# Optimization experiments

Measured on AMD Instinct MI355X. Metric: run time of the kernel, lower is better.

Reference implementation:

```python
import jax, jax.numpy as jnp
import numpy as np

LN_EPS = 1e-5

def layer_norm(x, w, b):
    m = jnp.mean(x, axis=-1, keepdims=True)
    v = jnp.mean((x - m) ** 2, axis=-1, keepdims=True)
    return (x - m) * jax.lax.rsqrt(v + LN_EPS) * w + b

def setup_inputs() -> dict:
    key = jax.random.key(0)
    ks = jax.random.split(key, 10)
    B, N, L = 32, 576, 100
    low, high = 1024, 1536
    inp = {
        "vit_feat": jax.random.normal(ks[0], (B, N, low), dtype=jnp.float32),
        "box_feat": jax.random.normal(ks[1], (B, L, high), dtype=jnp.float32),
        "lengths": jax.random.randint(ks[2], (B,), 0, L, dtype=jnp.int64),
        # query projector: LayerNorm(low) + Linear(low, low)
        "q_ln_w": jnp.ones((low,), jnp.float32),
        "q_ln_b": jnp.zeros((low,), jnp.float32),
        "q_w": jax.random.normal(ks[3], (low, low), dtype=jnp.float32) * 0.02,
        "q_b": jnp.zeros((low,), jnp.float32),
        # key projector: LayerNorm(high) + Linear(high, low)
        "k_ln_w": jnp.ones((high,), jnp.float32),
        "k_ln_b": jnp.zeros((high,), jnp.float32),
        "k_w": jax.random.normal(ks[4], (high, low), dtype=jnp.float32) * 0.02,
        "k_b": jnp.zeros((low,), jnp.float32),
        # value projector: LayerNorm(high) + Linear(high, low)
        "v_ln_w": jnp.ones((high,), jnp.float32),
        "v_ln_b": jnp.zeros((high,), jnp.float32),
        "v_w": jax.random.normal(ks[5], (high, low), dtype=jnp.float32) * 0.02,
        "v_b": jnp.zeros((low,), jnp.float32),
    }
    return inp

def reference(vit_feat, box_feat, lengths,
              q_ln_w, q_ln_b, q_w, q_b,
              k_ln_w, k_ln_b, k_w, k_b,
              v_ln_w, v_ln_b, v_w, v_b):
    B, L = box_feat.shape[0], box_feat.shape[1]
    # padding mask, same as the original per-row copy loop
    mask = jnp.arange(L)[None, :] < lengths[:, None]          # [B, L] bool
    q = layer_norm(vit_feat, q_ln_w, q_ln_b) @ q_w + q_b      # [B, N, low]
    k = layer_norm(box_feat, k_ln_w, k_ln_b) @ k_w + k_b      # [B, L, low]
    v = layer_norm(box_feat, v_ln_w, v_ln_b) @ v_w + v_b      # [B, L, low]
    scale = 1.0 / jnp.sqrt(jnp.asarray(k.shape[-1], q.dtype))
    att = jnp.einsum('bnd,bld->bnl', q, k * scale)            # [B, N, L]
    att = jnp.where(mask[:, None, :], att, -jnp.inf)
    att = jnp.nan_to_num(att)  # -inf -> finite min, matching torch nan_to_num
    att = jax.nn.softmax(att, axis=-1)
    out = jnp.einsum('bnl,bld->bnd', att, v)                  # [B, N, low]
    return vit_feat + out
```

## Files before the change

kernel.cpp:

```cpp
#include <hip/hip_runtime.h>
#include <stdint.h>

typedef __attribute__((ext_vector_type(8))) short short8;
typedef __attribute__((ext_vector_type(4))) float f32x4;

#define NEG_FLT_MAX (-3.402823466e38f)

__device__ __forceinline__ unsigned short f2bf(float f) {
  uint32_t u = __float_as_uint(f);
  uint32_t r = (u + 0x7fffu + ((u >> 16) & 1u)) >> 16;
  return (unsigned short)r;
}

__device__ __forceinline__ void gload16(const void* g, void* l) {
  __builtin_amdgcn_global_load_lds(
      (const __attribute__((address_space(1))) uint32_t*)g,
      (__attribute__((address_space(3))) uint32_t*)l, 16, 0, 0);
}

__global__ __launch_bounds__(256) void prep_kernel(
    const float* __restrict__ qw, const float* __restrict__ kw,
    const float* __restrict__ vw, const float* __restrict__ qb,
    const float* __restrict__ kb, float scale,
    unsigned short* __restrict__ qwb, unsigned short* __restrict__ kwb,
    unsigned short* __restrict__ vwt,
    float* __restrict__ bias3, float* __restrict__ w4, float* __restrict__ c4) {
  __shared__ float tile[32][33];
  const int bid = blockIdx.x;
  const int t = threadIdx.x;
  if (bid < 2560) {
    const int idx = bid * 256 + t;
    const int QG = 1024 * 1024 / 4;
    if (idx < QG) {
      float4 v = ((const float4*)qw)[idx];
      ushort4 o;
      o.x = f2bf(v.x); o.y = f2bf(v.y); o.z = f2bf(v.z); o.w = f2bf(v.w);
      ((ushort4*)qwb)[idx] = o;
    } else {
      const int j = idx - QG;
      float4 v = ((const float4*)kw)[j];
      ushort4 o;
      o.x = f2bf(v.x * scale); o.y = f2bf(v.y * scale);
      o.z = f2bf(v.z * scale); o.w = f2bf(v.w * scale);
      ((ushort4*)kwb)[j] = o;
    }
  } else if (bid < 4096) {
    const int j = bid - 2560;
    const int c0 = (j & 31) * 32, r0 = (j >> 5) * 32;
    const int tx = t & 31, ty = t >> 5;
#pragma unroll
    for (int i = ty; i < 32; i += 8)
      tile[i][tx] = vw[(size_t)(r0 + i) * 1024 + (c0 + tx)];
    __syncthreads();
#pragma unroll
    for (int i = ty; i < 32; i += 8)
      vwt[(size_t)(c0 + i) * 1536 + (r0 + tx)] = f2bf(tile[tx][i]);
  } else {
    const int idx = bid - 4096;
    const int wv = t >> 6, l = t & 63;
    float s = 0.f;
    if (idx < 256) {
      const int i = idx * 4 + wv;
      const float* row = qw + (size_t)i * 1024;
#pragma unroll
      for (int s0 = 0; s0 < 1024; s0 += 256) {
        float4 a = *(const float4*)(row + s0 + l * 4);
        float4 b = *(const float4*)(kb + s0 + l * 4);
        s += a.x * b.x + a.y * b.y + a.z * b.z + a.w * b.w;
      }
#pragma unroll
      for (int off = 32; off; off >>= 1) s += __shfl_xor(s, off);
      if (l == 0) bias3[i] = s * scale;
    } else if (idx < 640) {
      const int j = (idx - 256) * 4 + wv;
      const float* row = kw + (size_t)j * 1024;
#pragma unroll
      for (int s0 = 0; s0 < 1024; s0 += 256) {
        float4 a = *(const float4*)(row + s0 + l * 4);
        float4 b = *(const float4*)(qb + s0 + l * 4);
        s += a.x * b.x + a.y * b.y + a.z * b.z + a.w * b.w;
      }
#pragma unroll
      for (int off = 32; off; off >>= 1) s += __shfl_xor(s, off);
      if (l == 0) w4[j] = s * scale;
    } else if (wv == 0) {
#pragma unroll
      for (int s0 = 0; s0 < 1024; s0 += 256) {
        float4 a = *(const float4*)(qb + s0 + l * 4);
        float4 b = *(const float4*)(kb + s0 + l * 4);
        s += a.x * b.x + a.y * b.y + a.z * b.z + a.w * b.w;
      }
#pragma unroll
      for (int off = 32; off; off >>= 1) s += __shfl_xor(s, off);
      if (l == 0) *c4 = s * scale;
    }
  }
}

__device__ __forceinline__ void gemm_core64(
    const unsigned short* __restrict__ A, int lda, int rowmaxA, int tm0,
    const unsigned short* __restrict__ Bt, int ldb, int rowmaxB, int tn0,
    int K, unsigned short* As, unsigned short* Bs, f32x4 acc[4][4]) {
  const int tid = threadIdx.x;
  const int w = tid >> 6, l = tid & 63;
  const int wr = w >> 1, wc = w & 1;
  const int srow = (w << 4) + (l >> 2);
  const int scol = (l & 3) << 3;
  int ra0 = tm0 + srow;      if (ra0 > rowmaxA) ra0 = rowmaxA;
  int ra1 = tm0 + srow + 64; if (ra1 > rowmaxA) ra1 = rowmaxA;
  int rb0 = tn0 + srow;      if (rb0 > rowmaxB) rb0 = rowmaxB;
  int rb1 = tn0 + srow + 64; if (rb1 > rowmaxB) rb1 = rowmaxB;
  const unsigned short* pa0 = A + (size_t)ra0 * lda + scol;
  const unsigned short* pa1 = A + (size_t)ra1 * lda + scol;
  const unsigned short* pb0 = Bt + (size_t)rb0 * ldb + scol;
  const unsigned short* pb1 = Bt + (size_t)rb1 * ldb + scol;
  unsigned short* la0 = As + (w << 4) * 32;
  unsigned short* la1 = As + ((w << 4) + 64) * 32;
  unsigned short* lb0 = Bs + (w << 4) * 32;
  unsigned short* lb1 = Bs + ((w << 4) + 64) * 32;
  const int foff = ((l & 15) << 5) + ((l >> 4) << 3);
  const unsigned short* fa = As + (wr << 6) * 32 + foff;
  const unsigned short* fb = Bs + (wc << 6) * 32 + foff;
#pragma unroll
  for (int i = 0; i < 4; i++)
#pragma unroll
    for (int j = 0; j < 4; j++) acc[i][j] = (f32x4)0.0f;
  for (int k0 = 0; k0 < K; k0 += 64) {
    gload16(pa0 + k0, la0);
    gload16(pa1 + k0, la1);
    gload16(pb0 + k0, lb0);
    gload16(pb1 + k0, lb1);
    gload16(pa0 + k0 + 32, la0 + 4096);
    gload16(pa1 + k0 + 32, la1 + 4096);
    gload16(pb0 + k0 + 32, lb0 + 4096);
    gload16(pb1 + k0 + 32, lb1 + 4096);
    __syncthreads();
    {
      short8 a[4], b[4];
#pragma unroll
      for (int i = 0; i < 4; i++) a[i] = *(const short8*)(fa + i * 512);
#pragma unroll
      for (int j = 0; j < 4; j++) b[j] = *(const short8*)(fb + j * 512);
#pragma unroll
      for (int i = 0; i < 4; i++)
#pragma unroll
        for (int j = 0; j < 4; j++)
          acc[i][j] = __builtin_amdgcn_mfma_f32_16x16x32_bf16(a[i], b[j], acc[i][j], 0, 0, 0);
    }
    {
      short8 a[4], b[4];
#pragma unroll
      for (int i = 0; i < 4; i++) a[i] = *(const short8*)(fa + 4096 + i * 512);
#pragma unroll
      for (int j = 0; j < 4; j++) b[j] = *(const short8*)(fb + 4096 + j * 512);
#pragma unroll
      for (int i = 0; i < 4; i++)
#pragma unroll
        for (int j = 0; j < 4; j++)
          acc[i][j] = __builtin_amdgcn_mfma_f32_16x16x32_bf16(a[i], b[j], acc[i][j], 0, 0, 0);
    }
    __syncthreads();
  }
}

__global__ __launch_bounds__(256) void mid_kernel(
    const float* __restrict__ box,
    const float* __restrict__ klnw, const float* __restrict__ klnb,
    const float* __restrict__ vlnw, const float* __restrict__ vlnb,
    const unsigned short* __restrict__ qwb, const unsigned short* __restrict__ kwb,
    const float* __restrict__ w4v, const float* __restrict__ c4,
    unsigned short* __restrict__ kn, unsigned short* __restrict__ vn,
    unsigned short* __restrict__ W3, float* __restrict__ qbk) {
  __shared__ float red[8];
  __shared__ float redq[4];
  __shared__ unsigned short As[128 * 64];
  __shared__ unsigned short Bs[128 * 64];
  const int t = threadIdx.x;
  if (blockIdx.x < 3200) {
    const int row = blockIdx.x;
    const float4* xr = (const float4*)(box + (size_t)row * 1536);
    const float4 a = xr[t];
    float4 c = make_float4(0.f, 0.f, 0.f, 0.f);
    if (t < 128) c = xr[256 + t];
    float s = a.x + a.y + a.z + a.w + c.x + c.y + c.z + c.w;
    float ss = a.x * a.x + a.y * a.y + a.z * a.z + a.w * a.w +
               c.x * c.x + c.y * c.y + c.z * c.z + c.w * c.w;
#pragma unroll
    for (int off = 32; off > 0; off >>= 1) {
      s += __shfl_xor(s, off);
      ss += __shfl_xor(ss, off);
    }
    if ((t & 63) == 0) { red[(t >> 6) * 2] = s; red[(t >> 6) * 2 + 1] = ss; }
    __syncthreads();
    if (t == 0) {
      float aa = 0.f, bb = 0.f;
      for (int i = 0; i < 4; i++) { aa += red[i * 2]; bb += red[i * 2 + 1]; }
      red[0] = aa; red[1] = bb;
    }
    __syncthreads();
    s = red[0]; ss = red[1];
    const float m = s * (1.f / 1536.f);
    const float var = ss * (1.f / 1536.f) - m * m;
    const float rstd = rsqrtf(var + 1e-5f);
    float qd;
    {
      const float4 w4 = ((const float4*)klnw)[t];
      const float4 b4 = ((const float4*)klnb)[t];
      const float k0v = (a.x - m) * rstd * w4.x + b4.x;
      const float k1v = (a.y - m) * rstd * w4.y + b4.y;
      const float k2v = (a.z - m) * rstd * w4.z + b4.z;
      const float k3v = (a.w - m) * rstd * w4.w + b4.w;
      ushort4 o;
      o.x = f2bf(k0v); o.y = f2bf(k1v); o.z = f2bf(k2v); o.w = f2bf(k3v);
      ((ushort4*)(kn + (size_t)row * 1536))[t] = o;
      const float4 wq = ((const float4*)w4v)[t];
      qd = k0v * wq.x + k1v * wq.y + k2v * wq.z + k3v * wq.w;
      const float4 w4vv = ((const float4*)vlnw)[t];
      const float4 b4vv = ((const float4*)vlnb)[t];
      o.x = f2bf((a.x - m) * rstd * w4vv.x + b4vv.x);
      o.y = f2bf((a.y - m) * rstd * w4vv.y + b4vv.y);
      o.z = f2bf((a.z - m) * rstd * w4vv.z + b4vv.z);
      o.w = f2bf((a.w - m) * rstd * w4vv.w + b4vv.w);
      ((ushort4*)(vn + (size_t)row * 1536))[t] = o;
    }
    if (t < 128) {
      const int t2 = 256 + t;
      const float4 w4 = ((const float4*)klnw)[t2];
      const float4 b4 = ((const float4*)klnb)[t2];
      const float k0v = (c.x - m) * rstd * w4.x + b4.x;
      const float k1v = (c.y - m) * rstd * w4.y + b4.y;
      const float k2v = (c.z - m) * rstd * w4.z + b4.z;
      const float k3v = (c.w - m) * rstd * w4.w + b4.w;
      ushort4 o;
      o.x = f2bf(k0v); o.y = f2bf(k1v); o.z = f2bf(k2v); o.w = f2bf(k3v);
      ((ushort4*)(kn + (size_t)row * 1536))[t2] = o;
      const float4 wq = ((const float4*)w4v)[t2];
      qd += k0v * wq.x + k1v * wq.y + k2v * wq.z + k3v * wq.w;
      const float4 w4vv = ((const float4*)vlnw)[t2];
      const float4 b4vv = ((const float4*)vlnb)[t2];
      o.x = f2bf((c.x - m) * rstd * w4vv.x + b4vv.x);
      o.y = f2bf((c.y - m) * rstd * w4vv.y + b4vv.y);
      o.z = f2bf((c.z - m) * rstd * w4vv.z + b4vv.z);
      o.w = f2bf((c.w - m) * rstd * w4vv.w + b4vv.w);
      ((ushort4*)(vn + (size_t)row * 1536))[t2] = o;
    }
#pragma unroll
    for (int off = 32; off; off >>= 1) qd += __shfl_xor(qd, off);
    if ((t & 63) == 0) redq[t >> 6] = qd;
    __syncthreads();
    if (t == 0) qbk[row] = redq[0] + redq[1] + redq[2] + redq[3] + c4[0];
  } else {
    const int j = blockIdx.x - 3200;
    const int tm0 = (j & 7) * 128, tn0 = (j >> 3) * 128;
    f32x4 acc[4][4];
    gemm_core64(qwb, 1024, 1023, tm0, kwb, 1024, 1535, tn0, 1024, As, Bs, acc);
    const int w = t >> 6, l = t & 63;
    const int wr = w >> 1, wc = w & 1;
#pragma unroll
    for (int i = 0; i < 4; i++) {
      const int row0 = tm0 + wr * 64 + i * 16 + (l >> 4) * 4;
#pragma unroll
      for (int jj = 0; jj < 4; jj++) {
        const int col = tn0 + wc * 64 + jj * 16 + (l & 15);
#pragma unroll
        for (int r = 0; r < 4; r++)
          W3[(size_t)(row0 + r) * 1536 + col] = f2bf(acc[i][jj][r]);
      }
    }
  }
}

__global__ __launch_bounds__(256) void gemm_kv_kernel(
    const unsigned short* __restrict__ kn, const unsigned short* __restrict__ vn,
    const unsigned short* __restrict__ W3, const unsigned short* __restrict__ vwt,
    const float* __restrict__ bias3, const float* __restrict__ vb,
    unsigned short* __restrict__ kq, unsigned short* __restrict__ vT) {
  __shared__ unsigned short As[128 * 64];
  __shared__ unsigned short Bs[128 * 64];
  const int id = blockIdx.x;
  const int sw = (id & 7) * 50 + (id >> 3);
  const int z = sw / 200;
  const int rem = sw - z * 200;
  const int tm0 = (rem % 25) * 128, tn0 = (rem / 25) * 128;
  const unsigned short* A = z ? vn : kn;
  const unsigned short* Bt = z ? vwt : W3;
  const float* bias = z ? vb : bias3;
  f32x4 acc[4][4];
  gemm_core64(A, 1536, 3199, tm0, Bt, 1536, 1023, tn0, 1536, As, Bs, acc);
  const int tid = threadIdx.x;
  const int w = tid >> 6, l = tid & 63;
  const int wr = w >> 1, wc = w & 1;
#pragma unroll
  for (int i = 0; i < 4; i++) {
    const int row0 = tm0 + wr * 64 + i * 16 + (l >> 4) * 4;
#pragma unroll
    for (int j = 0; j < 4; j++) {
      const int col = tn0 + wc * 64 + j * 16 + (l & 15);
      const float bv = bias[col];
#pragma unroll
      for (int r = 0; r < 4; r++) {
        const int row = row0 + r;
        const float val = acc[i][j][r] + bv;
        if (!z) {
          kq[(size_t)row * 1024 + col] = f2bf(val);
        } else {
          const int bb = row / 100;
          const int ll = row - bb * 100;
          vT[((size_t)bb * 1024 + col) * 128 + ll] = f2bf(val);
        }
      }
    }
  }
}

__device__ __forceinline__ void block_reduce2(float& s, float& ss, float* red) {
#pragma unroll
  for (int off = 32; off > 0; off >>= 1) {
    s += __shfl_xor(s, off);
    ss += __shfl_xor(ss, off);
  }
  const int wave = threadIdx.x >> 6;
  const int lane = threadIdx.x & 63;
  if (lane == 0) { red[wave * 2] = s; red[wave * 2 + 1] = ss; }
  __syncthreads();
  if (threadIdx.x == 0) {
    float a = 0.f, b = 0.f;
    for (int i = 0; i < 4; i++) { a += red[i * 2]; b += red[i * 2 + 1]; }
    red[0] = a; red[1] = b;
  }
  __syncthreads();
  s = red[0]; ss = red[1];
}

__global__ __launch_bounds__(256) void ln_vit_kernel(
    const float* __restrict__ x, const float* __restrict__ w,
    const float* __restrict__ b, unsigned short* __restrict__ out) {
  __shared__ float red[8];
  const int row = blockIdx.x;
  const int t = threadIdx.x;
  const float4 v = ((const float4*)(x + (size_t)row * 1024))[t];
  float s = v.x + v.y + v.z + v.w;
  float ss = v.x * v.x + v.y * v.y + v.z * v.z + v.w * v.w;
  block_reduce2(s, ss, red);
  const float m = s * (1.f / 1024.f);
  const float var = ss * (1.f / 1024.f) - m * m;
  const float rstd = rsqrtf(var + 1e-5f);
  const float4 w4 = ((const float4*)w)[t];
  const float4 b4 = ((const float4*)b)[t];
  ushort4 o;
  o.x = f2bf((v.x - m) * rstd * w4.x + b4.x);
  o.y = f2bf((v.y - m) * rstd * w4.y + b4.y);
  o.z = f2bf((v.z - m) * rstd * w4.z + b4.z);
  o.w = f2bf((v.w - m) * rstd * w4.w + b4.w);
  ((ushort4*)(out + (size_t)row * 1024))[t] = o;
}

__global__ __launch_bounds__(256) void attfused_kernel(
    const unsigned short* __restrict__ qn, const unsigned short* __restrict__ kq,
    const unsigned short* __restrict__ vT, const float* __restrict__ qbk,
    const int* __restrict__ lengths, const float* __restrict__ vit,
    float* __restrict__ out) {
  __shared__ __align__(16) char smem[45824];
  float* Smat = (float*)smem;
  float* invr = (float*)(smem + 28672);
  float* qb_l = (float*)(smem + 28800);
  const int PB = 20480, BV = 29440;

  const int b = blockIdx.y;
  const int tm0 = blockIdx.x * 32;
  const int t = threadIdx.x;
  const int w = t >> 6, l = t & 63;
  const int lo = l & 15, hi = l >> 4;
  if (t < 128) qb_l[t] = (t < 100) ? qbk[b * 100 + t] : 0.f;

  const unsigned short* A = qn + (size_t)b * 576 * 1024;
  const unsigned short* B = kq + (size_t)b * 100 * 1024;
  const int ar = (t & 127) >> 2, ah = t >> 7, ac = (t & 3) << 3;
  const unsigned short* paA = A + (size_t)(tm0 + ar) * 1024 + ah * 32 + ac;
  const unsigned short* pbB[4];
#pragma unroll
  for (int i = 0; i < 4; i++) {
    int rb = (i & 1) * 64 + (t >> 2); if (rb > 99) rb = 99;
    pbB[i] = B + (size_t)rb * 1024 + (i >> 1) * 32 + ((t & 3) << 3);
  }
  const int cw = w << 5;

  f32x4 acc[2][2];
#pragma unroll
  for (int i = 0; i < 2; i++) { acc[i][0] = (f32x4)0.0f; acc[i][1] = (f32x4)0.0f; }

  for (int k0 = 0; k0 < 1024; k0 += 64) {
    gload16(paA + k0, smem + w * 1024);
#pragma unroll
    for (int i = 0; i < 4; i++)
      gload16(pbB[i] + k0, smem + 4096 + i * 4096 + w * 1024);
    __syncthreads();
#pragma unroll
    for (int half = 0; half < 2; half++) {
      short8 a[2], bb[2];
#pragma unroll
      for (int i = 0; i < 2; i++)
        a[i] = *(const short8*)(smem + half * 2048 + (i * 16 + lo) * 64 + hi * 16);
#pragma unroll
      for (int j = 0; j < 2; j++)
        bb[j] = *(const short8*)(smem + 4096 + half * 8192 + (cw + j * 16 + lo) * 64 + hi * 16);
#pragma unroll
      for (int i = 0; i < 2; i++)
#pragma unroll
        for (int j = 0; j < 2; j++)
          acc[i][j] = __builtin_amdgcn_mfma_f32_16x16x32_bf16(a[i], bb[j], acc[i][j], 0, 0, 0);
    }
    __syncthreads();
  }

#pragma unroll
  for (int i = 0; i < 2; i++) {
    const int r0 = i * 16 + hi * 4;
#pragma unroll
    for (int j = 0; j < 2; j++) {
      const int c = cw + j * 16 + lo;
      const float qb = qb_l[c];
#pragma unroll
      for (int rr = 0; rr < 4; rr++) Smat[c * 36 + r0 + rr] = acc[i][j][rr] + qb;
    }
  }
  __syncthreads();

  const int r = t >> 3, g = t & 7;
  const int len = lengths[b];
  float mx = NEG_FLT_MAX;
#pragma unroll
  for (int i = 0; i < 13; i++) {
    const int ll = g * 13 + i;
    if (ll < 100) {
      const float v = (ll < len) ? Smat[ll * 36 + r] : NEG_FLT_MAX;
      mx = fmaxf(mx, v);
    }
  }
  mx = fmaxf(mx, __shfl_xor(mx, 1));
  mx = fmaxf(mx, __shfl_xor(mx, 2));
  mx = fmaxf(mx, __shfl_xor(mx, 4));
  float sum = 0.f;
#pragma unroll
  for (int i = 0; i < 13; i++) {
    const int ll = g * 13 + i;
    if (ll < 100) {
      const float v = (ll < len) ? Smat[ll * 36 + r] : NEG_FLT_MAX;
      const float e = __expf(v - mx);
      Smat[ll * 36 + r] = e;
      sum += e;
    }
  }
  sum += __shfl_xor(sum, 1);
  sum += __shfl_xor(sum, 2);
  sum += __shfl_xor(sum, 4);
  if (g == 0) invr[r] = 1.f / sum;
  __syncthreads();

  {
    const float inv = invr[r];
#pragma unroll
    for (int jj = 0; jj < 4; jj++) {
      const int c0 = g * 16 + jj * 4;
      ushort4 o;
      o.x = (c0 + 0 < 100) ? f2bf(Smat[(c0 + 0) * 36 + r] * inv) : (unsigned short)0;
      o.y = (c0 + 1 < 100) ? f2bf(Smat[(c0 + 1) * 36 + r] * inv) : (unsigned short)0;
      o.z = (c0 + 2 < 100) ? f2bf(Smat[(c0 + 2) * 36 + r] * inv) : (unsigned short)0;
      o.w = (c0 + 3 < 100) ? f2bf(Smat[(c0 + 3) * 36 + r] * inv) : (unsigned short)0;
      const int phys = (r * 256 + g * 32 + jj * 8) ^ ((r & 7) << 4);
      *(ushort4*)(smem + PB + phys) = o;
    }
  }
  __syncthreads();

  const unsigned short* vTb = vT + (size_t)b * 131072;
  const float* vitb = vit + ((size_t)b * 576 + tm0) * 1024;
  float* outb = out + ((size_t)b * 576 + tm0) * 1024;
  const int sBcol = ((t & 15) ^ ((t >> 4) & 7)) << 3;
  for (int nt = 0; nt < 16; ++nt) {
#pragma unroll
    for (int i = 0; i < 4; i++) {
      const int vrow = nt * 64 + i * 16 + (t >> 4);
      gload16(vTb + (size_t)vrow * 128 + sBcol, smem + BV + i * 4096 + w * 1024);
    }
    __syncthreads();
    f32x4 acc2[2];
    acc2[0] = (f32x4)0.0f; acc2[1] = (f32x4)0.0f;
#pragma unroll
    for (int ks = 0; ks < 4; ks++) {
      short8 av[2], bv;
#pragma unroll
      for (int i = 0; i < 2; i++) {
        const int m = i * 16 + lo;
        av[i] = *(const short8*)(smem + PB + ((m * 256 + ks * 64 + hi * 16) ^ ((m & 7) << 4)));
      }
      const int n = (w << 4) + lo;
      bv = *(const short8*)(smem + BV + ((n * 256 + ks * 64 + hi * 16) ^ ((n & 7) << 4)));
      acc2[0] = __builtin_amdgcn_mfma_f32_16x16x32_bf16(av[0], bv, acc2[0], 0, 0, 0);
      acc2[1] = __builtin_amdgcn_mfma_f32_16x16x32_bf16(av[1], bv, acc2[1], 0, 0, 0);
    }
#pragma unroll
    for (int i = 0; i < 2; i++) {
      const int col = (w << 4) + lo;
#pragma unroll
      for (int rr = 0; rr < 4; rr++) {
        const int row = i * 16 + hi * 4 + rr;
        *(float*)(smem + ((row * 256 + col * 4) ^ ((row & 7) << 4))) = acc2[i][rr];
      }
    }
    __syncthreads();
#pragma unroll
    for (int m = 0; m < 2; m++) {
      const int row = m * 16 + (t >> 4);
      const int colb = (t & 15) * 4;
      float4 e = *(const float4*)(smem + ((row * 256 + colb * 4) ^ ((row & 7) << 4)));
      const size_t gidx = (size_t)row * 1024 + nt * 64 + colb;
      float4 vv = *(const float4*)(vitb + gidx);
      e.x += vv.x; e.y += vv.y; e.z += vv.z; e.w += vv.w;
      *(float4*)(outb + gidx) = e;
    }
    __syncthreads();
  }
}

extern "C" void kernel_launch(void* const* d_in, const int* in_sizes, int n_in,
                              void* d_out, int out_size, void* d_ws, size_t ws_size,
                              hipStream_t stream) {
  const float* vit = (const float*)d_in[0];
  const float* box = (const float*)d_in[1];
  const int* lengths = (const int*)d_in[2];
  const float* q_ln_w = (const float*)d_in[3];
  const float* q_ln_b = (const float*)d_in[4];
  const float* q_w = (const float*)d_in[5];
  const float* q_b = (const float*)d_in[6];
  const float* k_ln_w = (const float*)d_in[7];
  const float* k_ln_b = (const float*)d_in[8];
  const float* k_w = (const float*)d_in[9];
  const float* k_b = (const float*)d_in[10];
  const float* v_ln_w = (const float*)d_in[11];
  const float* v_ln_b = (const float*)d_in[12];
  const float* v_w = (const float*)d_in[13];
  const float* v_b = (const float*)d_in[14];
  float* out = (float*)d_out;
  char* ws = (char*)d_ws;

  unsigned short* kn    = (unsigned short*)(ws + 0);
  unsigned short* vn    = (unsigned short*)(ws + 9830400);
  unsigned short* v_wt  = (unsigned short*)(ws + 19660800);
  unsigned short* qwb   = (unsigned short*)(ws + 22806528);
  unsigned short* kwb   = (unsigned short*)(ws + 24903680);
  unsigned short* W3    = (unsigned short*)(ws + 28049408);
  float*          bias3 = (float*)(ws + 31195136);
  float*          w4    = (float*)(ws + 31199232);
  float*          c4    = (float*)(ws + 31207424);
  unsigned short* qn    = (unsigned short*)(ws + 0);
  float*          qbk   = (float*)(ws + 37748736);
  unsigned short* kq    = (unsigned short*)(ws + 37761536);
  unsigned short* vT    = (unsigned short*)(ws + 44315136);

  const float scale = 0.03125f;

  prep_kernel<<<4737, 256, 0, stream>>>(q_w, k_w, v_w, q_b, k_b, scale,
                                        qwb, kwb, v_wt, bias3, w4, c4);

  mid_kernel<<<3296, 256, 0, stream>>>(box, k_ln_w, k_ln_b, v_ln_w, v_ln_b,
                                       qwb, kwb, w4, c4, kn, vn, W3, qbk);

  gemm_kv_kernel<<<400, 256, 0, stream>>>(kn, vn, W3, v_wt, bias3, v_b, kq, vT);

  ln_vit_kernel<<<18432, 256, 0, stream>>>(vit, q_ln_w, q_ln_b, qn);

  attfused_kernel<<<dim3(18, 32), 256, 0, stream>>>(
      qn, kq, vT, qbk, lengths, vit, out);

  (void)in_sizes; (void)n_in; (void)out_size; (void)ws_size;
}
```

Baseline: 153.3 us.

## Merge weight prep into LayerNorm kernel and move qbk dot into KV GEMM launch

Removes the separate weight-prep kernel. The q_w/k_w bf16 conversion now happens inside the W3 GEMM tiles, with fp32 loaded and converted on the fly into LDS, and the v_w transpose and bias dots run as extra block ranges of one large kernel alongside the box LayerNorm. The per-row qbk dot product, previously fused into LayerNorm, now runs in extra blocks of the K/V GEMM kernel, reading bf16 kn. This cuts one launch and the intermediate qwb/kwb buffers. In exchange the W3 GEMM loses its async global-to-LDS loads, and qbk is computed from rounded bf16 activations.

```diff
diff --git a/kernel.cpp b/kernel.cpp
--- a/kernel.cpp
+++ b/kernel.cpp
@@ -12,89 +12,14 @@
   return (unsigned short)r;
 }
 
+__device__ __forceinline__ float bf2f(unsigned short u) {
+  return __uint_as_float(((uint32_t)u) << 16);
+}
+
 __device__ __forceinline__ void gload16(const void* g, void* l) {
   __builtin_amdgcn_global_load_lds(
       (const __attribute__((address_space(1))) uint32_t*)g,
       (__attribute__((address_space(3))) uint32_t*)l, 16, 0, 0);
-}
-
-__global__ __launch_bounds__(256) void prep_kernel(
-    const float* __restrict__ qw, const float* __restrict__ kw,
-    const float* __restrict__ vw, const float* __restrict__ qb,
-    const float* __restrict__ kb, float scale,
-    unsigned short* __restrict__ qwb, unsigned short* __restrict__ kwb,
-    unsigned short* __restrict__ vwt,
-    float* __restrict__ bias3, float* __restrict__ w4, float* __restrict__ c4) {
-  __shared__ float tile[32][33];
-  const int bid = blockIdx.x;
-  const int t = threadIdx.x;
-  if (bid < 2560) {
-    const int idx = bid * 256 + t;
-    const int QG = 1024 * 1024 / 4;
-    if (idx < QG) {
-      float4 v = ((const float4*)qw)[idx];
-      ushort4 o;
-      o.x = f2bf(v.x); o.y = f2bf(v.y); o.z = f2bf(v.z); o.w = f2bf(v.w);
-      ((ushort4*)qwb)[idx] = o;
-    } else {
-      const int j = idx - QG;
-      float4 v = ((const float4*)kw)[j];
-      ushort4 o;
-      o.x = f2bf(v.x * scale); o.y = f2bf(v.y * scale);
-      o.z = f2bf(v.z * scale); o.w = f2bf(v.w * scale);
-      ((ushort4*)kwb)[j] = o;
-    }
-  } else if (bid < 4096) {
-    const int j = bid - 2560;
-    const int c0 = (j & 31) * 32, r0 = (j >> 5) * 32;
-    const int tx = t & 31, ty = t >> 5;
-#pragma unroll
-    for (int i = ty; i < 32; i += 8)
-      tile[i][tx] = vw[(size_t)(r0 + i) * 1024 + (c0 + tx)];
-    __syncthreads();
-#pragma unroll
-    for (int i = ty; i < 32; i += 8)
-      vwt[(size_t)(c0 + i) * 1536 + (r0 + tx)] = f2bf(tile[tx][i]);
-  } else {
-    const int idx = bid - 4096;
-    const int wv = t >> 6, l = t & 63;
-    float s = 0.f;
-    if (idx < 256) {
-      const int i = idx * 4 + wv;
-      const float* row = qw + (size_t)i * 1024;
-#pragma unroll
-      for (int s0 = 0; s0 < 1024; s0 += 256) {
-        float4 a = *(const float4*)(row + s0 + l * 4);
-        float4 b = *(const float4*)(kb + s0 + l * 4);
-        s += a.x * b.x + a.y * b.y + a.z * b.z + a.w * b.w;
-      }
-#pragma unroll
-      for (int off = 32; off; off >>= 1) s += __shfl_xor(s, off);
-      if (l == 0) bias3[i] = s * scale;
-    } else if (idx < 640) {
-      const int j = (idx - 256) * 4 + wv;
-      const float* row = kw + (size_t)j * 1024;
-#pragma unroll
-      for (int s0 = 0; s0 < 1024; s0 += 256) {
-        float4 a = *(const float4*)(row + s0 + l * 4);
-        float4 b = *(const float4*)(qb + s0 + l * 4);
-        s += a.x * b.x + a.y * b.y + a.z * b.z + a.w * b.w;
-      }
-#pragma unroll
-      for (int off = 32; off; off >>= 1) s += __shfl_xor(s, off);
-      if (l == 0) w4[j] = s * scale;
-    } else if (wv == 0) {
-#pragma unroll
-      for (int s0 = 0; s0 < 1024; s0 += 256) {
-        float4 a = *(const float4*)(qb + s0 + l * 4);
-        float4 b = *(const float4*)(kb + s0 + l * 4);
-        s += a.x * b.x + a.y * b.y + a.z * b.z + a.w * b.w;
-      }
-#pragma unroll
-      for (int off = 32; off; off >>= 1) s += __shfl_xor(s, off);
-      if (l == 0) *c4 = s * scale;
-    }
-  }
 }
 
 __device__ __forceinline__ void gemm_core64(
@@ -163,21 +88,22 @@
   }
 }
 
-__global__ __launch_bounds__(256) void mid_kernel(
+__global__ __launch_bounds__(256) void mega_kernel(
     const float* __restrict__ box,
     const float* __restrict__ klnw, const float* __restrict__ klnb,
     const float* __restrict__ vlnw, const float* __restrict__ vlnb,
-    const unsigned short* __restrict__ qwb, const unsigned short* __restrict__ kwb,
-    const float* __restrict__ w4v, const float* __restrict__ c4,
+    const float* __restrict__ qw, const float* __restrict__ kw,
+    const float* __restrict__ vw, const float* __restrict__ qb,
+    const float* __restrict__ kb, float scale,
     unsigned short* __restrict__ kn, unsigned short* __restrict__ vn,
-    unsigned short* __restrict__ W3, float* __restrict__ qbk) {
-  __shared__ float red[8];
-  __shared__ float redq[4];
-  __shared__ unsigned short As[128 * 64];
-  __shared__ unsigned short Bs[128 * 64];
+    unsigned short* __restrict__ W3, unsigned short* __restrict__ vwt,
+    float* __restrict__ bias3, float* __restrict__ w4, float* __restrict__ c4) {
+  __shared__ __align__(16) char mshm[32896];
+  const int bid = blockIdx.x;
   const int t = threadIdx.x;
-  if (blockIdx.x < 3200) {
-    const int row = blockIdx.x;
+  if (bid < 3200) {
+    float* red = (float*)mshm;
+    const int row = bid;
     const float4* xr = (const float4*)(box + (size_t)row * 1536);
     const float4 a = xr[t];
     float4 c = make_float4(0.f, 0.f, 0.f, 0.f);
@@ -202,60 +128,115 @@
     const float m = s * (1.f / 1536.f);
     const float var = ss * (1.f / 1536.f) - m * m;
     const float rstd = rsqrtf(var + 1e-5f);
-    float qd;
     {
-      const float4 w4 = ((const float4*)klnw)[t];
+      const float4 w4v = ((const float4*)klnw)[t];
       const float4 b4 = ((const float4*)klnb)[t];
-      const float k0v = (a.x - m) * rstd * w4.x + b4.x;
-      const float k1v = (a.y - m) * rstd * w4.y + b4.y;
-      const float k2v = (a.z - m) * rstd * w4.z + b4.z;
-      const float k3v = (a.w - m) * rstd * w4.w + b4.w;
       ushort4 o;
-      o.x = f2bf(k0v); o.y = f2bf(k1v); o.z = f2bf(k2v); o.w = f2bf(k3v);
+      o.x = f2bf((a.x - m) * rstd * w4v.x + b4.x);
+      o.y = f2bf((a.y - m) * rstd * w4v.y + b4.y);
+      o.z = f2bf((a.z - m) * rstd * w4v.z + b4.z);
+      o.w = f2bf((a.w - m) * rstd * w4v.w + b4.w);
       ((ushort4*)(kn + (size_t)row * 1536))[t] = o;
-      const float4 wq = ((const float4*)w4v)[t];
-      qd = k0v * wq.x + k1v * wq.y + k2v * wq.z + k3v * wq.w;
-      const float4 w4vv = ((const float4*)vlnw)[t];
-      const float4 b4vv = ((const float4*)vlnb)[t];
-      o.x = f2bf((a.x - m) * rstd * w4vv.x + b4vv.x);
-      o.y = f2bf((a.y - m) * rstd * w4vv.y + b4vv.y);
-      o.z = f2bf((a.z - m) * rstd * w4vv.z + b4vv.z);
-      o.w = f2bf((a.w - m) * rstd * w4vv.w + b4vv.w);
+      const float4 wv2 = ((const float4*)vlnw)[t];
+      const float4 bv2 = ((const float4*)vlnb)[t];
+      o.x = f2bf((a.x - m) * rstd * wv2.x + bv2.x);
+      o.y = f2bf((a.y - m) * rstd * wv2.y + bv2.y);
+      o.z = f2bf((a.z - m) * rstd * wv2.z + bv2.z);
+      o.w = f2bf((a.w - m) * rstd * wv2.w + bv2.w);
       ((ushort4*)(vn + (size_t)row * 1536))[t] = o;
     }
     if (t < 128) {
       const int t2 = 256 + t;
-      const float4 w4 = ((const float4*)klnw)[t2];
+      const float4 w4v = ((const float4*)klnw)[t2];
       const float4 b4 = ((const float4*)klnb)[t2];
-      const float k0v = (c.x - m) * rstd * w4.x + b4.x;
-      const float k1v = (c.y - m) * rstd * w4.y + b4.y;
-      const float k2v = (c.z - m) * rstd * w4.z + b4.z;
-      const float k3v = (c.w - m) * rstd * w4.w + b4.w;
       ushort4 o;
-      o.x = f2bf(k0v); o.y = f2bf(k1v); o.z = f2bf(k2v); o.w = f2bf(k3v);
+      o.x = f2bf((c.x - m) * rstd * w4v.x + b4.x);
+      o.y = f2bf((c.y - m) * rstd * w4v.y + b4.y);
+      o.z = f2bf((c.z - m) * rstd * w4v.z + b4.z);
+      o.w = f2bf((c.w - m) * rstd * w4v.w + b4.w);
       ((ushort4*)(kn + (size_t)row * 1536))[t2] = o;
-      const float4 wq = ((const float4*)w4v)[t2];
-      qd += k0v * wq.x + k1v * wq.y + k2v * wq.z + k3v * wq.w;
-      const float4 w4vv = ((const float4*)vlnw)[t2];
-      const float4 b4vv = ((const float4*)vlnb)[t2];
-      o.x = f2bf((c.x - m) * rstd * w4vv.x + b4vv.x);
-      o.y = f2bf((c.y - m) * rstd * w4vv.y + b4vv.y);
-      o.z = f2bf((c.z - m) * rstd * w4vv.z + b4vv.z);
-      o.w = f2bf((c.w - m) * rstd * w4vv.w + b4vv.w);
+      const float4 wv2 = ((const float4*)vlnw)[t2];
+      const float4 bv2 = ((const float4*)vlnb)[t2];
+      o.x = f2bf((c.x - m) * rstd * wv2.x + bv2.x);
+      o.y = f2bf((c.y - m) * rstd * wv2.y + bv2.y);
+      o.z = f2bf((c.z - m) * rstd * wv2.z + bv2.z);
+      o.w = f2bf((c.w - m) * rstd * wv2.w + bv2.w);
       ((ushort4*)(vn + (size_t)row * 1536))[t2] = o;
     }
-#pragma unroll
-    for (int off = 32; off; off >>= 1) qd += __shfl_xor(qd, off);
-    if ((t & 63) == 0) redq[t >> 6] = qd;
-    __syncthreads();
-    if (t == 0) qbk[row] = redq[0] + redq[1] + redq[2] + redq[3] + c4[0];
-  } else {
-    const int j = blockIdx.x - 3200;
+  } else if (bid < 3296) {
+    unsigned short* As = (unsigned short*)mshm;
+    unsigned short* Bs = As + 8192;
+    const int j = bid - 3200;
     const int tm0 = (j & 7) * 128, tn0 = (j >> 3) * 128;
-    f32x4 acc[4][4];
-    gemm_core64(qwb, 1024, 1023, tm0, kwb, 1024, 1535, tn0, 1024, As, Bs, acc);
     const int w = t >> 6, l = t & 63;
     const int wr = w >> 1, wc = w & 1;
+    const int srow = (w << 4) + (l >> 2);
+    const int scol = (l & 3) << 3;
+    const float* pa0 = qw + (size_t)(tm0 + srow) * 1024 + scol;
+    const float* pa1 = pa0 + 64 * 1024;
+    const float* pb0 = kw + (size_t)(tn0 + srow) * 1024 + scol;
+    const float* pb1 = pb0 + 64 * 1024;
+    unsigned short* da0 = As + srow * 32 + scol;
+    unsigned short* da1 = As + (srow + 64) * 32 + scol;
+    unsigned short* db0 = Bs + srow * 32 + scol;
+    unsigned short* db1 = Bs + (srow + 64) * 32 + scol;
+    const int foff = ((l & 15) << 5) + ((l >> 4) << 3);
+    const unsigned short* fa = As + (wr << 6) * 32 + foff;
+    const unsigned short* fb = Bs + (wc << 6) * 32 + foff;
+    f32x4 acc[4][4];
+#pragma unroll
+    for (int i = 0; i < 4; i++)
+#pragma unroll
+      for (int jj = 0; jj < 4; jj++) acc[i][jj] = (f32x4)0.0f;
+
+#define CVT8(src, dst, scl) do {                                              \
+      float4 x0_ = *(const float4*)(src);                                     \
+      float4 x1_ = *(const float4*)((src) + 4);                               \
+      short8 pk_;                                                             \
+      pk_[0] = (short)f2bf(x0_.x * (scl)); pk_[1] = (short)f2bf(x0_.y * (scl)); \
+      pk_[2] = (short)f2bf(x0_.z * (scl)); pk_[3] = (short)f2bf(x0_.w * (scl)); \
+      pk_[4] = (short)f2bf(x1_.x * (scl)); pk_[5] = (short)f2bf(x1_.y * (scl)); \
+      pk_[6] = (short)f2bf(x1_.z * (scl)); pk_[7] = (short)f2bf(x1_.w * (scl)); \
+      *(short8*)(dst) = pk_;                                                  \
+    } while (0)
+
+    for (int k0 = 0; k0 < 1024; k0 += 64) {
+      CVT8(pa0 + k0, da0, 1.0f);
+      CVT8(pa1 + k0, da1, 1.0f);
+      CVT8(pb0 + k0, db0, scale);
+      CVT8(pb1 + k0, db1, scale);
+      CVT8(pa0 + k0 + 32, da0 + 4096, 1.0f);
+      CVT8(pa1 + k0 + 32, da1 + 4096, 1.0f);
+      CVT8(pb0 + k0 + 32, db0 + 4096, scale);
+      CVT8(pb1 + k0 + 32, db1 + 4096, scale);
+      __syncthreads();
+      {
+        short8 a[4], b[4];
+#pragma unroll
+        for (int i = 0; i < 4; i++) a[i] = *(const short8*)(fa + i * 512);
+#pragma unroll
+        for (int jj = 0; jj < 4; jj++) b[jj] = *(const short8*)(fb + jj * 512);
+#pragma unroll
+        for (int i = 0; i < 4; i++)
+#pragma unroll
+          for (int jj = 0; jj < 4; jj++)
+            acc[i][jj] = __builtin_amdgcn_mfma_f32_16x16x32_bf16(a[i], b[jj], acc[i][jj], 0, 0, 0);
+      }
+      {
+        short8 a[4], b[4];
+#pragma unroll
+        for (int i = 0; i < 4; i++) a[i] = *(const short8*)(fa + 4096 + i * 512);
+#pragma unroll
+        for (int jj = 0; jj < 4; jj++) b[jj] = *(const short8*)(fb + 4096 + jj * 512);
+#pragma unroll
+        for (int i = 0; i < 4; i++)
+#pragma unroll
+          for (int jj = 0; jj < 4; jj++)
+            acc[i][jj] = __builtin_amdgcn_mfma_f32_16x16x32_bf16(a[i], b[jj], acc[i][jj], 0, 0, 0);
+      }
+      __syncthreads();
+    }
+#undef CVT8
 #pragma unroll
     for (int i = 0; i < 4; i++) {
       const int row0 = tm0 + wr * 64 + i * 16 + (l >> 4) * 4;
@@ -267,69 +248,124 @@
           W3[(size_t)(row0 + r) * 1536 + col] = f2bf(acc[i][jj][r]);
       }
     }
-  }
-}
-
-__global__ __launch_bounds__(256) void gemm_kv_kernel(
+  } else if (bid < 4832) {
+    float* tile = (float*)mshm;
+    const int j = bid - 3296;
+    const int c0 = (j & 31) * 32, r0 = (j >> 5) * 32;
+    const int tx = t & 31, ty = t >> 5;
+#pragma unroll
+    for (int i = ty; i < 32; i += 8)
+      tile[i * 33 + tx] = vw[(size_t)(r0 + i) * 1024 + (c0 + tx)];
+    __syncthreads();
+#pragma unroll
+    for (int i = ty; i < 32; i += 8)
+      vwt[(size_t)(c0 + i) * 1536 + (r0 + tx)] = f2bf(tile[tx * 33 + i]);
+  } else {
+    const int idx = bid - 4832;
+    const int wv = t >> 6, l = t & 63;
+    float s = 0.f;
+    if (idx < 256) {
+      const int i = idx * 4 + wv;
+      const float* row = qw + (size_t)i * 1024;
+#pragma unroll
+      for (int s0 = 0; s0 < 1024; s0 += 256) {
+        float4 a = *(const float4*)(row + s0 + l * 4);
+        float4 b = *(const float4*)(kb + s0 + l * 4);
+        s += a.x * b.x + a.y * b.y + a.z * b.z + a.w * b.w;
+      }
+#pragma unroll
+      for (int off = 32; off; off >>= 1) s += __shfl_xor(s, off);
+      if (l == 0) bias3[i] = s * scale;
+    } else if (idx < 640) {
+      const int j = (idx - 256) * 4 + wv;
+      const float* row = kw + (size_t)j * 1024;
+#pragma unroll
+      for (int s0 = 0; s0 < 1024; s0 += 256) {
+        float4 a = *(const float4*)(row + s0 + l * 4);
+        float4 b = *(const float4*)(qb + s0 + l * 4);
+        s += a.x * b.x + a.y * b.y + a.z * b.z + a.w * b.w;
+      }
+#pragma unroll
+      for (int off = 32; off; off >>= 1) s += __shfl_xor(s, off);
+      if (l == 0) w4[j] = s * scale;
+    } else if (wv == 0) {
+#pragma unroll
+      for (int s0 = 0; s0 < 1024; s0 += 256) {
+        float4 a = *(const float4*)(qb + s0 + l * 4);
+        float4 b = *(const float4*)(kb + s0 + l * 4);
+        s += a.x * b.x + a.y * b.y + a.z * b.z + a.w * b.w;
+      }
+#pragma unroll
+      for (int off = 32; off; off >>= 1) s += __shfl_xor(s, off);
+      if (l == 0) *c4 = s * scale;
+    }
+  }
+}
+
+__global__ __launch_bounds__(256) void kvq_kernel(
     const unsigned short* __restrict__ kn, const unsigned short* __restrict__ vn,
     const unsigned short* __restrict__ W3, const unsigned short* __restrict__ vwt,
     const float* __restrict__ bias3, const float* __restrict__ vb,
-    unsigned short* __restrict__ kq, unsigned short* __restrict__ vT) {
+    const float* __restrict__ w4, const float* __restrict__ c4,
+    unsigned short* __restrict__ kq, unsigned short* __restrict__ vT,
+    float* __restrict__ qbk) {
   __shared__ unsigned short As[128 * 64];
   __shared__ unsigned short Bs[128 * 64];
-  const int id = blockIdx.x;
-  const int sw = (id & 7) * 50 + (id >> 3);
-  const int z = sw / 200;
-  const int rem = sw - z * 200;
-  const int tm0 = (rem % 25) * 128, tn0 = (rem / 25) * 128;
-  const unsigned short* A = z ? vn : kn;
-  const unsigned short* Bt = z ? vwt : W3;
-  const float* bias = z ? vb : bias3;
-  f32x4 acc[4][4];
-  gemm_core64(A, 1536, 3199, tm0, Bt, 1536, 1023, tn0, 1536, As, Bs, acc);
-  const int tid = threadIdx.x;
-  const int w = tid >> 6, l = tid & 63;
-  const int wr = w >> 1, wc = w & 1;
-#pragma unroll
-  for (int i = 0; i < 4; i++) {
-    const int row0 = tm0 + wr * 64 + i * 16 + (l >> 4) * 4;
-#pragma unroll
-    for (int j = 0; j < 4; j++) {
-      const int col = tn0 + wc * 64 + j * 16 + (l & 15);
-      const float bv = bias[col];
-#pragma unroll
-      for (int r = 0; r < 4; r++) {
-        const int row = row0 + r;
-        const float val = acc[i][j][r] + bv;
-        if (!z) {
-          kq[(size_t)row * 1024 + col] = f2bf(val);
-        } else {
-          const int bb = row / 100;
-          const int ll = row - bb * 100;
-          vT[((size_t)bb * 1024 + col) * 128 + ll] = f2bf(val);
+  const int bid = blockIdx.x;
+  if (bid < 400) {
+    const int sw = (bid & 7) * 50 + (bid >> 3);
+    const int z = sw / 200;
+    const int rem = sw - z * 200;
+    const int tm0 = (rem % 25) * 128, tn0 = (rem / 25) * 128;
+    const unsigned short* A = z ? vn : kn;
+    const unsigned short* Bt = z ? vwt : W3;
+    const float* bias = z ? vb : bias3;
+    f32x4 acc[4][4];
+    gemm_core64(A, 1536, 3199, tm0, Bt, 1536, 1023, tn0, 1536, As, Bs, acc);
+    const int tid = threadIdx.x;
+    const int w = tid >> 6, l = tid & 63;
+    const int wr = w >> 1, wc = w & 1;
+#pragma unroll
+    for (int i = 0; i < 4; i++) {
+      const int row0 = tm0 + wr * 64 + i * 16 + (l >> 4) * 4;
+#pragma unroll
+      for (int j = 0; j < 4; j++) {
+        const int col = tn0 + wc * 64 + j * 16 + (l & 15);
+        const float bv = bias[col];
+#pragma unroll
+        for (int r = 0; r < 4; r++) {
+          const int row = row0 + r;
+          const float val = acc[i][j][r] + bv;
+          if (!z) {
+            kq[(size_t)row * 1024 + col] = f2bf(val);
+          } else {
+            const int bb = row / 100;
+            const int ll = row - bb * 100;
+            vT[((size_t)bb * 1024 + col) * 128 + ll] = f2bf(val);
+          }
         }
       }
     }
-  }
-}
-
-__device__ __forceinline__ void block_reduce2(float& s, float& ss, float* red) {
-#pragma unroll
-  for (int off = 32; off > 0; off >>= 1) {
-    s += __shfl_xor(s, off);
-    ss += __shfl_xor(ss, off);
-  }
-  const int wave = threadIdx.x >> 6;
-  const int lane = threadIdx.x & 63;
-  if (lane == 0) { red[wave * 2] = s; red[wave * 2 + 1] = ss; }
-  __syncthreads();
-  if (threadIdx.x == 0) {
-    float a = 0.f, b = 0.f;
-    for (int i = 0; i < 4; i++) { a += red[i * 2]; b += red[i * 2 + 1]; }
-    red[0] = a; red[1] = b;
-  }
-  __syncthreads();
-  s = red[0]; ss = red[1];
+  } else {
+    const int wv = threadIdx.x >> 6, l = threadIdx.x & 63;
+    const int row = (bid - 400) * 4 + wv;
+    const unsigned short* r = kn + (size_t)row * 1536;
+    float s = 0.f;
+#pragma unroll
+    for (int s0 = 0; s0 < 1536; s0 += 512) {
+      short8 v = *(const short8*)(r + s0 + l * 8);
+      const float* wp = w4 + s0 + l * 8;
+      float4 w0 = *(const float4*)wp;
+      float4 w1 = *(const float4*)(wp + 4);
+      s += bf2f((unsigned short)v[0]) * w0.x + bf2f((unsigned short)v[1]) * w0.y +
+           bf2f((unsigned short)v[2]) * w0.z + bf2f((unsigned short)v[3]) * w0.w +
+           bf2f((unsigned short)v[4]) * w1.x + bf2f((unsigned short)v[5]) * w1.y +
+           bf2f((unsigned short)v[6]) * w1.z + bf2f((unsigned short)v[7]) * w1.w;
+    }
+#pragma unroll
+    for (int off = 32; off; off >>= 1) s += __shfl_xor(s, off);
+    if (l == 0) qbk[row] = s + *c4;
+  }
 }
 
 __global__ __launch_bounds__(256) void ln_vit_kernel(
@@ -341,7 +377,20 @@
   const float4 v = ((const float4*)(x + (size_t)row * 1024))[t];
   float s = v.x + v.y + v.z + v.w;
   float ss = v.x * v.x + v.y * v.y + v.z * v.z + v.w * v.w;
-  block_reduce2(s, ss, red);
+#pragma unroll
+  for (int off = 32; off > 0; off >>= 1) {
+    s += __shfl_xor(s, off);
+    ss += __shfl_xor(ss, off);
+  }
+  if ((t & 63) == 0) { red[(t >> 6) * 2] = s; red[(t >> 6) * 2 + 1] = ss; }
+  __syncthreads();
+  if (t == 0) {
+    float a = 0.f, b2 = 0.f;
+    for (int i = 0; i < 4; i++) { a += red[i * 2]; b2 += red[i * 2 + 1]; }
+    red[0] = a; red[1] = b2;
+  }
+  __syncthreads();
+  s = red[0]; ss = red[1];
   const float m = s * (1.f / 1024.f);
   const float var = ss * (1.f / 1024.f) - m * m;
   const float rstd = rsqrtf(var + 1e-5f);
@@ -547,8 +596,6 @@
   unsigned short* kn    = (unsigned short*)(ws + 0);
   unsigned short* vn    = (unsigned short*)(ws + 9830400);
   unsigned short* v_wt  = (unsigned short*)(ws + 19660800);
-  unsigned short* qwb   = (unsigned short*)(ws + 22806528);
-  unsigned short* kwb   = (unsigned short*)(ws + 24903680);
   unsigned short* W3    = (unsigned short*)(ws + 28049408);
   float*          bias3 = (float*)(ws + 31195136);
   float*          w4    = (float*)(ws + 31199232);
@@ -560,13 +607,12 @@
 
   const float scale = 0.03125f;
 
-  prep_kernel<<<4737, 256, 0, stream>>>(q_w, k_w, v_w, q_b, k_b, scale,
-                                        qwb, kwb, v_wt, bias3, w4, c4);
-
-  mid_kernel<<<3296, 256, 0, stream>>>(box, k_ln_w, k_ln_b, v_ln_w, v_ln_b,
-                                       qwb, kwb, w4, c4, kn, vn, W3, qbk);
-
-  gemm_kv_kernel<<<400, 256, 0, stream>>>(kn, vn, W3, v_wt, bias3, v_b, kq, vT);
+  mega_kernel<<<5473, 256, 0, stream>>>(
+      box, k_ln_w, k_ln_b, v_ln_w, v_ln_b, q_w, k_w, v_w, q_b, k_b, scale,
+      kn, vn, W3, v_wt, bias3, w4, c4);
+
+  kvq_kernel<<<1200, 256, 0, stream>>>(
+      kn, vn, W3, v_wt, bias3, v_b, w4, c4, kq, vT, qbk);
 
   ln_vit_kernel<<<18432, 256, 0, stream>>>(vit, q_ln_w, q_ln_b, qn);
 
```

Result: slower. 160.9 us (+4.9%).
